# Performance work log

Measured on AMD Instinct MI355X. Metric: run time of the kernel, lower is better.

## Reference

```python
import jax, jax.numpy as jnp
import numpy as np

N = 8192
D = 64  # node feature width
E = 64  # edge-derived feature width


def setup_inputs() -> dict:
    key = jax.random.key(0)
    k1, k2, k3 = jax.random.split(key, 3)
    # Dense normalized adjacency (module stores normalize(A).toarray()); values in [0,1).
    A = jax.random.uniform(k1, (N, N), dtype=jnp.float32) / N  # scaled like a normalized adjacency
    F = jax.random.normal(k2, (N, D), dtype=jnp.float32)
    new_features = jax.random.normal(k3, (N, E), dtype=jnp.float32)
    return {"A": A, "F": F, "new_features": new_features}


def reference(A, F, new_features):
    # layer 1: node branch gets ReLU, edge-feature branch does not
    h = jax.nn.relu(A @ F)              # [N, D]
    g = A @ new_features                # [N, E]
    # layer 2
    h = jax.nn.relu(A @ h)              # [N, D]
    g = A @ g                           # [N, E]
    return jnp.concatenate([h, g], axis=-1)  # [N, D+E]
```

## Files before the change

### kernel.cpp

```cpp
#include <hip/hip_runtime.h>
#include <hip/hip_bf16.h>


typedef unsigned short ushort_t;
typedef __attribute__((ext_vector_type(8))) short short8;
typedef __attribute__((ext_vector_type(4))) float f32x4;
typedef __attribute__((ext_vector_type(4))) unsigned short us4;

#define NN 8192
#define NO 128
#define BKK 64
#define NSPLIT 8
#define KSPAN (NN / NSPLIT)
#define GITERS (KSPAN / BKK)

__global__ void detect_dtype(const ushort_t* __restrict__ A, int* __restrict__ flag) {
  __shared__ int smax, szero;
  const int t = threadIdx.x;
  if (t == 0) { smax = 0; szero = 0; }
  __syncthreads();
  int lmax = 0, lzero = 0;
  #pragma unroll
  for (int j = 0; j < 8; ++j) {
    int idx = t * 8 + j;
    int u = (int)A[idx];
    if ((idx & 1) == 0) {
      lmax = max(lmax, u);
      lzero += (u == 0) ? 1 : 0;
    }
  }
  atomicMax(&smax, lmax);
  atomicAdd(&szero, lzero);
  __syncthreads();
  if (t == 0) *flag = (smax > 0x3A00 || szero > 800) ? 1 : 0;
}

__global__ void zero_ws(float* __restrict__ p) {
  size_t i = ((size_t)blockIdx.x * 256 + threadIdx.x) * 4;
  *(float4*)(p + i) = make_float4(0.f, 0.f, 0.f, 0.f);
}

__device__ __forceinline__ short bf16bits(float x) {
  __hip_bfloat16 h = __float2bfloat16(x);
  return *reinterpret_cast<short*>(&h);
}

__device__ __forceinline__ short8 cvt8(float4 a, float4 b) {
  short8 r;
  r[0] = bf16bits(a.x); r[1] = bf16bits(a.y); r[2] = bf16bits(a.z); r[3] = bf16bits(a.w);
  r[4] = bf16bits(b.x); r[5] = bf16bits(b.y); r[6] = bf16bits(b.z); r[7] = bf16bits(b.w);
  return r;
}

__device__ __forceinline__ void gl2lds16(const ushort_t* g, ushort_t* l) {
  __builtin_amdgcn_global_load_lds(
      (const __attribute__((address_space(1))) void*)g,
      (__attribute__((address_space(3))) void*)l, 16, 0, 0);
}

__global__ void pack_bt(const ushort_t* __restrict__ F, const ushort_t* __restrict__ NF,
                        ushort_t* __restrict__ Bt, const int* __restrict__ flag) {
  int idx = blockIdx.x * 256 + threadIdx.x;
  int n = idx >> 10;
  int k0 = (idx & 1023) << 3;
  ushort_t* dst = Bt + ((size_t)n << 13) + k0;
  if (*flag) {
    const float* src = (n < 64) ? ((const float*)F + n) : ((const float*)NF + (n - 64));
    #pragma unroll
    for (int j = 0; j < 8; ++j) dst[j] = (ushort_t)bf16bits(src[(size_t)(k0 + j) << 6]);
  } else {
    const ushort_t* src = (n < 64) ? (F + n) : (NF + (n - 64));
    #pragma unroll
    for (int j = 0; j < 8; ++j) dst[j] = src[(size_t)(k0 + j) << 6];
  }
}

__device__ __forceinline__ void compute_tile(const ushort_t* bA, const ushort_t* bB,
                                             int w, int lane, f32x4 (&acc)[4][2]) {
  #pragma unroll
  for (int s = 0; s < 2; ++s) {
    short8 b0 = *(const short8*)(bB + (4 * w + s) * 512 + lane * 8);
    short8 b1 = *(const short8*)(bB + (4 * w + 2 + s) * 512 + lane * 8);
    #pragma unroll
    for (int mt = 0; mt < 4; ++mt) {
      short8 a = *(const short8*)(bA + (2 * mt + s) * 512 + lane * 8);
      acc[mt][0] = __builtin_amdgcn_mfma_f32_16x16x32_bf16(a, b0, acc[mt][0], 0, 0, 0);
      acc[mt][1] = __builtin_amdgcn_mfma_f32_16x16x32_bf16(a, b1, acc[mt][1], 0, 0, 0);
    }
  }
}

__global__ __launch_bounds__(256) void gemm_atomic(
    const ushort_t* __restrict__ Au, const float* __restrict__ Af,
    ushort_t* __restrict__ Abf, const ushort_t* __restrict__ Bt,
    float* __restrict__ P, const int* __restrict__ flag, int wb, int rdabf) {
  __shared__ __align__(16) ushort_t lsA[8 * 512];
  __shared__ __align__(16) ushort_t lsB[16 * 512];
  const int t = threadIdx.x;
  const int w = t >> 6, lane = t & 63;
  const int mtile = blockIdx.x >> 3;
  const int split = blockIdx.x & 7;
  const size_t m0 = (size_t)mtile * 64;
  const int kb = split * KSPAN;

  const int wh = w >> 1, ws_ = w & 1;
  const int l15 = lane & 15, lq = lane >> 4;
  const size_t rowA0 = m0 + (size_t)wh * 16 + l15;
  const size_t colb = (size_t)kb + ws_ * 32 + lq * 8;
  const size_t offA0 = rowA0 * NN + colb;
  const size_t offA1 = offA0 + (size_t)32 * NN;
  const ushort_t* gB0 = Bt + ((size_t)wh * 16 + l15) * NN + colb;

  const f32x4 zero = {0.f, 0.f, 0.f, 0.f};
  f32x4 acc[4][2];
  #pragma unroll
  for (int mt = 0; mt < 4; ++mt) { acc[mt][0] = zero; acc[mt][1] = zero; }

  const int fl = *flag;

  if (fl && !rdabf) {
    const float* gA0f = Af + offA0;
    const float* gA1f = Af + offA1;
    ushort_t* pW0 = Abf + offA0;
    ushort_t* pW1 = Abf + offA1;
    for (int it = 0; it < GITERS; ++it) {
      float4 a00 = *(const float4*)gA0f;
      float4 a01 = *(const float4*)(gA0f + 4);
      float4 a10 = *(const float4*)gA1f;
      float4 a11 = *(const float4*)(gA1f + 4);
      short8 rb0 = *(const short8*)gB0;
      short8 rb1 = *(const short8*)(gB0 + (size_t)32 * NN);
      short8 rb2 = *(const short8*)(gB0 + (size_t)64 * NN);
      short8 rb3 = *(const short8*)(gB0 + (size_t)96 * NN);
      gA0f += BKK; gA1f += BKK; gB0 += BKK;
      short8 c0 = cvt8(a00, a01);
      short8 c1 = cvt8(a10, a11);
      if (wb) {
        *(short8*)pW0 = c0;
        *(short8*)pW1 = c1;
        pW0 += BKK; pW1 += BKK;
      }
      *(short8*)(lsA + t * 8) = c0;
      *(short8*)(lsA + t * 8 + 2048) = c1;
      *(short8*)(lsB + t * 8) = rb0;
      *(short8*)(lsB + t * 8 + 2048) = rb1;
      *(short8*)(lsB + t * 8 + 4096) = rb2;
      *(short8*)(lsB + t * 8 + 6144) = rb3;
      __syncthreads();
      compute_tile(lsA, lsB, w, lane, acc);
      __syncthreads();
    }
  } else {
    const ushort_t* Ab = rdabf ? (const ushort_t*)Abf : Au;
    const ushort_t* gA0 = Ab + offA0;
    const ushort_t* gA1 = Ab + offA1;
    ushort_t* dA0 = lsA + w * 512;
    ushort_t* dA1 = lsA + w * 512 + 2048;
    ushort_t* dB  = lsB + w * 512;
    for (int it = 0; it < GITERS; ++it) {
      gl2lds16(gA0, dA0);
      gl2lds16(gA1, dA1);
      #pragma unroll
      for (int j = 0; j < 4; ++j)
        gl2lds16(gB0 + (size_t)(32 * j) * NN, dB + j * 2048);
      gA0 += BKK; gA1 += BKK; gB0 += BKK;
      __syncthreads();
      compute_tile(lsA, lsB, w, lane, acc);
      __syncthreads();
    }
  }

  const int cn0 = 32 * w + l15;
  const int rb = lq * 4;
  #pragma unroll
  for (int mt = 0; mt < 4; ++mt) {
    float* dst = P + (m0 + mt * 16 + rb) * NO;
    #pragma unroll
    for (int reg = 0; reg < 4; ++reg) {
      unsafeAtomicAdd(&dst[(size_t)reg * NO + cn0], acc[mt][0][reg]);
      unsafeAtomicAdd(&dst[(size_t)reg * NO + cn0 + 16], acc[mt][1][reg]);
    }
  }
}

__global__ void epi_t(const float* __restrict__ P, ushort_t* __restrict__ Ct) {
  __shared__ ushort_t lt[128 * 65];
  const size_t base = (size_t)blockIdx.x * (64 * NO);
  const int t = threadIdx.x;
  for (int i = 0; i < 32; ++i) {
    int e = i * 256 + t;
    int n = e & 127, m = e >> 7;
    float v = P[base + e];
    if (n < 64) v = fmaxf(v, 0.f);
    lt[n * 65 + m] = (ushort_t)bf16bits(v);
  }
  __syncthreads();
  const int n = t >> 1, h = t & 1;
  const size_t m0 = (size_t)blockIdx.x * 64;
  ushort_t* dst = Ct + (size_t)n * NN + m0 + h * 32;
  #pragma unroll
  for (int jj = 0; jj < 4; ++jj) {
    short8 v;
    #pragma unroll
    for (int j = 0; j < 8; ++j) v[j] = (short)lt[n * 65 + h * 32 + jj * 8 + j];
    *(short8*)(dst + jj * 8) = v;
  }
}

__global__ void epi_out(const float* __restrict__ P, ushort_t* __restrict__ outb,
                        float* __restrict__ outf, const int* __restrict__ flag) {
  int idx = blockIdx.x * 256 + threadIdx.x;
  size_t e = (size_t)idx * 4;
  float4 v = *(const float4*)(P + e);
  float s[4] = {v.x, v.y, v.z, v.w};
  int n0 = (int)(e & 127);
  #pragma unroll
  for (int j = 0; j < 4; ++j) if (n0 + j < 64) s[j] = fmaxf(s[j], 0.f);
  if (*flag) {
    *(float4*)(outf + e) = make_float4(s[0], s[1], s[2], s[3]);
  } else {
    us4 r;
    #pragma unroll
    for (int j = 0; j < 4; ++j) r[j] = (ushort_t)bf16bits(s[j]);
    *(us4*)(outb + e) = r;
  }
}

extern "C" void kernel_launch(void* const* d_in, const int* in_sizes, int n_in,
                              void* d_out, int out_size, void* d_ws, size_t ws_size,
                              hipStream_t stream) {
  const ushort_t* A  = (const ushort_t*)d_in[0];
  const ushort_t* F  = (const ushort_t*)d_in[1];
  const ushort_t* NF = (const ushort_t*)d_in[2];

  char* ws = (char*)d_ws;
  ushort_t* Bt = (ushort_t*)(ws);
  ushort_t* Ct = (ushort_t*)(ws + (2u << 20));
  float*    P1 = (float*)(ws + (4u << 20));
  float*    P2 = (float*)(ws + (8u << 20));
  int*    flag = (int*)(ws + (12u << 20));
  ushort_t* Abf = (ushort_t*)(ws + (16u << 20));

  const int wsok = (ws_size >= ((size_t)144 << 20)) ? 1 : 0;

  detect_dtype<<<1, 256, 0, stream>>>(A, flag);
  zero_ws<<<2048, 256, 0, stream>>>(P1);
  pack_bt<<<512, 256, 0, stream>>>(F, NF, Bt, flag);
  gemm_atomic<<<1024, 256, 0, stream>>>(A, (const float*)A, Abf, Bt, P1, flag,
                                        wsok, 0);
  epi_t<<<128, 256, 0, stream>>>(P1, Ct);
  gemm_atomic<<<1024, 256, 0, stream>>>(A, (const float*)A, Abf, Ct, P2, flag,
                                        0, wsok);
  epi_out<<<1024, 256, 0, stream>>>(P2, (ushort_t*)d_out, (float*)d_out, flag);
}
```

Baseline: 493.2 us.

## Replace LDS-staged GEMM with direct global fragment loads per wave

Rewrites the split-K GEMM so each wave loads its MFMA A and B fragments straight from global memory instead of staging tiles through shared memory with block barriers. Each wave covers 16 rows and all 128 output columns, stepping 32 along K. This removes LDS traffic and __syncthreads stalls, but B fragments are now fetched by every wave and rely on cache reuse. The rdabf path is also gated on the dtype flag.

```diff
diff --git a/kernel.cpp b/kernel.cpp
--- a/kernel.cpp
+++ b/kernel.cpp
@@ -9,10 +9,9 @@
 
 #define NN 8192
 #define NO 128
-#define BKK 64
 #define NSPLIT 8
 #define KSPAN (NN / NSPLIT)
-#define GITERS (KSPAN / BKK)
+#define KSTEPS (KSPAN / 32)
 
 __global__ void detect_dtype(const ushort_t* __restrict__ A, int* __restrict__ flag) {
   __shared__ int smax, szero;
@@ -50,12 +49,6 @@
   r[0] = bf16bits(a.x); r[1] = bf16bits(a.y); r[2] = bf16bits(a.z); r[3] = bf16bits(a.w);
   r[4] = bf16bits(b.x); r[5] = bf16bits(b.y); r[6] = bf16bits(b.z); r[7] = bf16bits(b.w);
   return r;
-}
-
-__device__ __forceinline__ void gl2lds16(const ushort_t* g, ushort_t* l) {
-  __builtin_amdgcn_global_load_lds(
-      (const __attribute__((address_space(1))) void*)g,
-      (__attribute__((address_space(3))) void*)l, 16, 0, 0);
 }
 
 __global__ void pack_bt(const ushort_t* __restrict__ F, const ushort_t* __restrict__ NF,
@@ -75,110 +68,79 @@
   }
 }
 
-__device__ __forceinline__ void compute_tile(const ushort_t* bA, const ushort_t* bB,
-                                             int w, int lane, f32x4 (&acc)[4][2]) {
-  #pragma unroll
-  for (int s = 0; s < 2; ++s) {
-    short8 b0 = *(const short8*)(bB + (4 * w + s) * 512 + lane * 8);
-    short8 b1 = *(const short8*)(bB + (4 * w + 2 + s) * 512 + lane * 8);
-    #pragma unroll
-    for (int mt = 0; mt < 4; ++mt) {
-      short8 a = *(const short8*)(bA + (2 * mt + s) * 512 + lane * 8);
-      acc[mt][0] = __builtin_amdgcn_mfma_f32_16x16x32_bf16(a, b0, acc[mt][0], 0, 0, 0);
-      acc[mt][1] = __builtin_amdgcn_mfma_f32_16x16x32_bf16(a, b1, acc[mt][1], 0, 0, 0);
-    }
-  }
-}
-
-__global__ __launch_bounds__(256) void gemm_atomic(
+__global__ __launch_bounds__(256) void gemm_frag(
     const ushort_t* __restrict__ Au, const float* __restrict__ Af,
     ushort_t* __restrict__ Abf, const ushort_t* __restrict__ Bt,
     float* __restrict__ P, const int* __restrict__ flag, int wb, int rdabf) {
-  __shared__ __align__(16) ushort_t lsA[8 * 512];
-  __shared__ __align__(16) ushort_t lsB[16 * 512];
   const int t = threadIdx.x;
   const int w = t >> 6, lane = t & 63;
-  const int mtile = blockIdx.x >> 3;
+  const int mblk = blockIdx.x >> 3;
   const int split = blockIdx.x & 7;
-  const size_t m0 = (size_t)mtile * 64;
+  const int l15 = lane & 15, lq = lane >> 4;
   const int kb = split * KSPAN;
-
-  const int wh = w >> 1, ws_ = w & 1;
-  const int l15 = lane & 15, lq = lane >> 4;
-  const size_t rowA0 = m0 + (size_t)wh * 16 + l15;
-  const size_t colb = (size_t)kb + ws_ * 32 + lq * 8;
-  const size_t offA0 = rowA0 * NN + colb;
-  const size_t offA1 = offA0 + (size_t)32 * NN;
-  const ushort_t* gB0 = Bt + ((size_t)wh * 16 + l15) * NN + colb;
+  const size_t row = (size_t)mblk * 64 + w * 16 + l15;
+  const size_t offA = row * NN + kb + lq * 8;
+  const ushort_t* bp = Bt + (size_t)l15 * NN + kb + lq * 8;
 
   const f32x4 zero = {0.f, 0.f, 0.f, 0.f};
-  f32x4 acc[4][2];
-  #pragma unroll
-  for (int mt = 0; mt < 4; ++mt) { acc[mt][0] = zero; acc[mt][1] = zero; }
+  f32x4 acc[8];
+  #pragma unroll
+  for (int nt = 0; nt < 8; ++nt) acc[nt] = zero;
 
   const int fl = *flag;
 
   if (fl && !rdabf) {
-    const float* gA0f = Af + offA0;
-    const float* gA1f = Af + offA1;
-    ushort_t* pW0 = Abf + offA0;
-    ushort_t* pW1 = Abf + offA1;
-    for (int it = 0; it < GITERS; ++it) {
-      float4 a00 = *(const float4*)gA0f;
-      float4 a01 = *(const float4*)(gA0f + 4);
-      float4 a10 = *(const float4*)gA1f;
-      float4 a11 = *(const float4*)(gA1f + 4);
-      short8 rb0 = *(const short8*)gB0;
-      short8 rb1 = *(const short8*)(gB0 + (size_t)32 * NN);
-      short8 rb2 = *(const short8*)(gB0 + (size_t)64 * NN);
-      short8 rb3 = *(const short8*)(gB0 + (size_t)96 * NN);
-      gA0f += BKK; gA1f += BKK; gB0 += BKK;
-      short8 c0 = cvt8(a00, a01);
-      short8 c1 = cvt8(a10, a11);
-      if (wb) {
-        *(short8*)pW0 = c0;
-        *(short8*)pW1 = c1;
-        pW0 += BKK; pW1 += BKK;
+    const float* ap = Af + offA;
+    ushort_t* wp = Abf + offA;
+    if (wb) {
+      #pragma unroll 2
+      for (int it = 0; it < KSTEPS; ++it) {
+        float4 x0 = *(const float4*)ap;
+        float4 x1 = *(const float4*)(ap + 4);
+        short8 a = cvt8(x0, x1);
+        *(short8*)wp = a;
+        #pragma unroll
+        for (int nt = 0; nt < 8; ++nt) {
+          short8 b = *(const short8*)(bp + (size_t)(nt * 16) * NN);
+          acc[nt] = __builtin_amdgcn_mfma_f32_16x16x32_bf16(a, b, acc[nt], 0, 0, 0);
+        }
+        ap += 32; wp += 32; bp += 32;
       }
-      *(short8*)(lsA + t * 8) = c0;
-      *(short8*)(lsA + t * 8 + 2048) = c1;
-      *(short8*)(lsB + t * 8) = rb0;
-      *(short8*)(lsB + t * 8 + 2048) = rb1;
-      *(short8*)(lsB + t * 8 + 4096) = rb2;
-      *(short8*)(lsB + t * 8 + 6144) = rb3;
-      __syncthreads();
-      compute_tile(lsA, lsB, w, lane, acc);
-      __syncthreads();
+    } else {
+      #pragma unroll 2
+      for (int it = 0; it < KSTEPS; ++it) {
+        float4 x0 = *(const float4*)ap;
+        float4 x1 = *(const float4*)(ap + 4);
+        short8 a = cvt8(x0, x1);
+        #pragma unroll
+        for (int nt = 0; nt < 8; ++nt) {
+          short8 b = *(const short8*)(bp + (size_t)(nt * 16) * NN);
+          acc[nt] = __builtin_amdgcn_mfma_f32_16x16x32_bf16(a, b, acc[nt], 0, 0, 0);
+        }
+        ap += 32; bp += 32;
+      }
     }
   } else {
-    const ushort_t* Ab = rdabf ? (const ushort_t*)Abf : Au;
-    const ushort_t* gA0 = Ab + offA0;
-    const ushort_t* gA1 = Ab + offA1;
-    ushort_t* dA0 = lsA + w * 512;
-    ushort_t* dA1 = lsA + w * 512 + 2048;
-    ushort_t* dB  = lsB + w * 512;
-    for (int it = 0; it < GITERS; ++it) {
-      gl2lds16(gA0, dA0);
-      gl2lds16(gA1, dA1);
+    const ushort_t* Ab = (rdabf && fl) ? (const ushort_t*)Abf : Au;
+    const ushort_t* ap = Ab + offA;
+    #pragma unroll 2
+    for (int it = 0; it < KSTEPS; ++it) {
+      short8 a = *(const short8*)ap;
       #pragma unroll
-      for (int j = 0; j < 4; ++j)
-        gl2lds16(gB0 + (size_t)(32 * j) * NN, dB + j * 2048);
-      gA0 += BKK; gA1 += BKK; gB0 += BKK;
-      __syncthreads();
-      compute_tile(lsA, lsB, w, lane, acc);
-      __syncthreads();
-    }
-  }
-
-  const int cn0 = 32 * w + l15;
-  const int rb = lq * 4;
-  #pragma unroll
-  for (int mt = 0; mt < 4; ++mt) {
-    float* dst = P + (m0 + mt * 16 + rb) * NO;
+      for (int nt = 0; nt < 8; ++nt) {
+        short8 b = *(const short8*)(bp + (size_t)(nt * 16) * NN);
+        acc[nt] = __builtin_amdgcn_mfma_f32_16x16x32_bf16(a, b, acc[nt], 0, 0, 0);
+      }
+      ap += 32; bp += 32;
+    }
+  }
+
+  const size_t m0 = (size_t)mblk * 64 + w * 16 + lq * 4;
+  #pragma unroll
+  for (int nt = 0; nt < 8; ++nt) {
     #pragma unroll
     for (int reg = 0; reg < 4; ++reg) {
-      unsafeAtomicAdd(&dst[(size_t)reg * NO + cn0], acc[mt][0][reg]);
-      unsafeAtomicAdd(&dst[(size_t)reg * NO + cn0 + 16], acc[mt][1][reg]);
+      unsafeAtomicAdd(&P[(m0 + reg) * NO + nt * 16 + l15], acc[nt][reg]);
     }
   }
 }
@@ -246,10 +208,10 @@
   detect_dtype<<<1, 256, 0, stream>>>(A, flag);
   zero_ws<<<2048, 256, 0, stream>>>(P1);
   pack_bt<<<512, 256, 0, stream>>>(F, NF, Bt, flag);
-  gemm_atomic<<<1024, 256, 0, stream>>>(A, (const float*)A, Abf, Bt, P1, flag,
-                                        wsok, 0);
+  gemm_frag<<<1024, 256, 0, stream>>>(A, (const float*)A, Abf, Bt, P1, flag,
+                                      wsok, 0);
   epi_t<<<128, 256, 0, stream>>>(P1, Ct);
-  gemm_atomic<<<1024, 256, 0, stream>>>(A, (const float*)A, Abf, Ct, P2, flag,
-                                        0, wsok);
+  gemm_frag<<<1024, 256, 0, stream>>>(A, (const float*)A, Abf, Ct, P2, flag,
+                                      0, wsok);
   epi_out<<<1024, 256, 0, stream>>>(P2, (ushort_t*)d_out, (float*)d_out, flag);
 }
```

Measured after the change: 655.4 us. 1.33x slower.
